# Performance work log

Measured on AMD Instinct MI355X. Metric: run time of the kernel, lower is better.

## Reference

```python
import jax, jax.numpy as jnp
import numpy as np

B, T, E, H = 16, 1024, 1024, 16
DH = E // H  # 64, divisible by 4
THETA = 10000.0


def setup_inputs() -> dict:
    key = jax.random.key(0)
    ks = jax.random.split(key, 10)
    inp = {
        "hidden_states": jax.random.normal(ks[0], (B, T, E), dtype=jnp.float32),
        "rope_pos": jax.random.randint(ks[1], (B, T, 2), 0, 32, dtype=jnp.int32),
    }
    s = 0.02
    inp["Wq"] = jax.random.normal(ks[2], (E, E), dtype=jnp.float32) * s
    inp["bq"] = jnp.zeros((E,), dtype=jnp.float32)
    inp["Wk"] = jax.random.normal(ks[3], (E, E), dtype=jnp.float32) * s
    inp["bk"] = jnp.zeros((E,), dtype=jnp.float32)
    inp["Wv"] = jax.random.normal(ks[4], (E, E), dtype=jnp.float32) * s
    inp["bv"] = jnp.zeros((E,), dtype=jnp.float32)
    inp["Wo"] = jax.random.normal(ks[5], (E, E), dtype=jnp.float32) * s
    inp["bo"] = jnp.zeros((E,), dtype=jnp.float32)
    return inp


def _rotate_half(x):
    # interleaved pairs: (x0,x1,x2,x3,...) -> (-x1,x0,-x3,x2,...)
    x_even = x[..., ::2]
    x_odd = x[..., 1::2]
    return jnp.stack((-x_odd, x_even), axis=-1).reshape(x.shape)


def _apply_rope_2d(q, k, rope_pos, theta):
    Dh = q.shape[-1]
    half, quarter = Dh // 2, Dh // 4
    dtype = q.dtype
    idx = jnp.arange(quarter, dtype=dtype)
    inv = (theta ** (-2.0 * idx / quarter)).astype(dtype)  # [quarter]
    pos_h = rope_pos[..., 0].astype(dtype)[..., None]  # [B,T,1]
    pos_w = rope_pos[..., 1].astype(dtype)[..., None]
    ang_h = pos_h * inv  # [B,T,quarter]
    ang_w = pos_w * inv
    ri = lambda a: jnp.repeat(a, 2, axis=-1)[:, None]  # -> [B,1,T,half]
    cos_h, sin_h = ri(jnp.cos(ang_h)), ri(jnp.sin(ang_h))
    cos_w, sin_w = ri(jnp.cos(ang_w)), ri(jnp.sin(ang_w))
    q_h, q_w = q[..., :half], q[..., half:]
    k_h, k_w = k[..., :half], k[..., half:]
    q_h = q_h * cos_h + _rotate_half(q_h) * sin_h
    k_h = k_h * cos_h + _rotate_half(k_h) * sin_h
    q_w = q_w * cos_w + _rotate_half(q_w) * sin_w
    k_w = k_w * cos_w + _rotate_half(k_w) * sin_w
    return jnp.concatenate([q_h, q_w], axis=-1), jnp.concatenate([k_h, k_w], axis=-1)


def reference(hidden_states, rope_pos, Wq, bq, Wk, bk, Wv, bv, Wo, bo):
    b, t, e = hidden_states.shape
    scale = DH ** -0.5
    # torch nn.Linear: y = x @ W.T + b, W is [out, in]
    proj = lambda x, W, bias: jnp.einsum('bte,oe->bto', x, W) + bias
    q = proj(hidden_states, Wq, bq).reshape(b, t, H, DH).transpose(0, 2, 1, 3)
    k = proj(hidden_states, Wk, bk).reshape(b, t, H, DH).transpose(0, 2, 1, 3)
    v = proj(hidden_states, Wv, bv).reshape(b, t, H, DH).transpose(0, 2, 1, 3)
    q, k = _apply_rope_2d(q, k, rope_pos, THETA)
    # eager attention: scores in input dtype, softmax in float32
    scores = jnp.einsum('bhqd,bhkd->bhqk', q, k) * scale
    w = jax.nn.softmax(scores.astype(jnp.float32), axis=-1).astype(q.dtype)
    out = jnp.einsum('bhqk,bhkd->bhqd', w, v)
    out = out.transpose(0, 2, 1, 3).reshape(b, t, e)
    return jnp.einsum('bte,oe->bto', out, Wo) + bo
```

## Files before the change

kernel.cpp:

```cpp
#include <hip/hip_runtime.h>
#include <hip/hip_bf16.h>

#define B_  16
#define T_  1024
#define E_  1024
#define H_  16
#define DH_ 64

typedef short s16x8 __attribute__((ext_vector_type(8)));
typedef float f32x4 __attribute__((ext_vector_type(4)));
typedef unsigned short u16x4 __attribute__((ext_vector_type(4)));

__device__ __forceinline__ void async_cp16(const void* g, void* l) {
  __builtin_amdgcn_global_load_lds(
      (__attribute__((address_space(1))) unsigned int*)(g),
      (__attribute__((address_space(3))) unsigned int*)(l), 16, 0, 0);
}

__device__ __forceinline__ s16x8 frag8(const void* p) { return *(const s16x8*)p; }

__device__ __forceinline__ float fexp2(float x) {
#if __has_builtin(__builtin_amdgcn_exp2f)
  return __builtin_amdgcn_exp2f(x);
#else
  return exp2f(x);
#endif
}

__device__ __forceinline__ unsigned short f2bu(float x) {
  __hip_bfloat16 h = __float2bfloat16(x);
  return *reinterpret_cast<unsigned short*>(&h);
}

__global__ __launch_bounds__(256) void cast_f32_bf16(const float* __restrict__ in,
                                                     __hip_bfloat16* __restrict__ out,
                                                     int n4) {
  int i = blockIdx.x * 256 + threadIdx.x;
  if (i >= n4) return;
  float4 v = ((const float4*)in)[i];
  __hip_bfloat16* o = out + (size_t)i * 4;
  o[0] = __float2bfloat16(v.x);
  o[1] = __float2bfloat16(v.y);
  o[2] = __float2bfloat16(v.z);
  o[3] = __float2bfloat16(v.w);
}

#define GEMM_CORE(A_, B_PTR_, K_)                                              \
  __shared__ __align__(16) __hip_bfloat16 As[128 * 64];                        \
  __shared__ __align__(16) __hip_bfloat16 Bs[128 * 64];                        \
  const int tid  = threadIdx.x;                                                \
  const int lane = tid & 63, wave = tid >> 6;                                  \
  const int col  = lane & 15, quad = lane >> 4;                                \
  const int wm = (wave >> 1) << 6, wn = (wave & 1) << 6;                       \
  const f32x4 fzero = {0.f, 0.f, 0.f, 0.f};                                    \
  f32x4 acc[4][4];                                                             \
  _Pragma("unroll") for (int i = 0; i < 4; i++)                                \
    _Pragma("unroll") for (int j = 0; j < 4; j++) acc[i][j] = fzero;           \
  const int r8 = lane >> 3;                                                    \
  const int kgs = (lane & 7) ^ (r8 & 7);                                       \
  const char* Asrc[4]; const char* Bsrc[4]; char* Adst[4]; char* Bdst[4];      \
  _Pragma("unroll") for (int u = 0; u < 4; u++) {                              \
    int ch = u * 4 + wave;                                                     \
    int row = ch * 8 + r8;                                                     \
    Asrc[u] = (const char*)(A_ + (size_t)(bm + row) * K_) + kgs * 16;          \
    Bsrc[u] = (const char*)(B_PTR_ + (size_t)(bn + row) * K_) + kgs * 16;      \
    Adst[u] = (char*)As + ch * 1024;                                           \
    Bdst[u] = (char*)Bs + ch * 1024;                                           \
  }                                                                            \
  const int sw0 = ((quad) ^ (col & 7)) * 16;                                   \
  const int sw1 = ((quad + 4) ^ (col & 7)) * 16;                               \
  for (int kt = 0; kt < (K_ >> 6); ++kt) {                                     \
    __syncthreads();                                                           \
    const int koff = kt * 128;                                                 \
    _Pragma("unroll") for (int u = 0; u < 4; u++) {                            \
      async_cp16(Asrc[u] + koff, Adst[u]);                                     \
      async_cp16(Bsrc[u] + koff, Bdst[u]);                                     \
    }                                                                          \
    __syncthreads();                                                           \
    s16x8 af[2][4], bf[2][4];                                                  \
    _Pragma("unroll") for (int i = 0; i < 4; i++) {                            \
      af[0][i] = frag8((const char*)As + (wm + i * 16 + col) * 128 + sw0);     \
      af[1][i] = frag8((const char*)As + (wm + i * 16 + col) * 128 + sw1);     \
    }                                                                          \
    _Pragma("unroll") for (int j = 0; j < 4; j++) {                            \
      bf[0][j] = frag8((const char*)Bs + (wn + j * 16 + col) * 128 + sw0);     \
      bf[1][j] = frag8((const char*)Bs + (wn + j * 16 + col) * 128 + sw1);     \
    }                                                                          \
    _Pragma("unroll") for (int i = 0; i < 4; i++)                              \
      _Pragma("unroll") for (int j = 0; j < 4; j++) {                          \
        acc[i][j] = __builtin_amdgcn_mfma_f32_16x16x32_bf16(af[0][i], bf[0][j], acc[i][j], 0, 0, 0); \
        acc[i][j] = __builtin_amdgcn_mfma_f32_16x16x32_bf16(af[1][i], bf[1][j], acc[i][j], 0, 0, 0); \
      }                                                                        \
  }

__global__ __launch_bounds__(256, 2) void gemm_qkv(const __hip_bfloat16* __restrict__ A,
                                                   const __hip_bfloat16* __restrict__ Wqkv,
                                                   const float* __restrict__ bq,
                                                   const float* __restrict__ bk,
                                                   const float* __restrict__ bv,
                                                   __hip_bfloat16* __restrict__ Qb,
                                                   __hip_bfloat16* __restrict__ Kb,
                                                   __hip_bfloat16* __restrict__ Vt) {
  const int bm = (blockIdx.x & 127) << 7;
  const int bn = (blockIdx.x >> 7) << 7;
  GEMM_CORE(A, Wqkv, 1024)

  const int seg = bn >> 10;
  const float* bp = (seg == 0) ? bq : (seg == 1) ? bk : bv;
  float bcol[4];
#pragma unroll
  for (int j = 0; j < 4; j++) bcol[j] = bp[(bn & 1023) + wn + j * 16 + col];
#pragma unroll
  for (int i = 0; i < 4; i++) {
#pragma unroll
    for (int j = 0; j < 4; j++) {
      const int nc = (bn & 1023) + wn + j * 16 + col;
#pragma unroll
      for (int r = 0; r < 4; r++) {
        const int grow = bm + wm + i * 16 + quad * 4 + r;
        float v = acc[i][j][r] + bcol[j];
        if (seg == 0) {
          Qb[(size_t)grow * 1024 + nc] = __float2bfloat16(v);
        } else if (seg == 1) {
          Kb[(size_t)grow * 1024 + nc] = __float2bfloat16(v);
        } else {
          int bb = grow >> 10, tt = grow & 1023;
          int hh = nc >> 6, dd = nc & 63;
          Vt[(((size_t)bb * H_ + hh) * DH_ + dd) * T_ + tt] = __float2bfloat16(v);
        }
      }
    }
  }
}

__global__ __launch_bounds__(256, 2) void gemm_out(const __hip_bfloat16* __restrict__ A,
                                                   const __hip_bfloat16* __restrict__ Bw,
                                                   const float* __restrict__ bias,
                                                   float* __restrict__ Cout) {
  const int bm = (blockIdx.x & 127) << 7;
  const int bn = (blockIdx.x >> 7) << 7;
  GEMM_CORE(A, Bw, 1024)

  float bcol[4];
#pragma unroll
  for (int j = 0; j < 4; j++) bcol[j] = bias[bn + wn + j * 16 + col];
#pragma unroll
  for (int i = 0; i < 4; i++)
#pragma unroll
    for (int j = 0; j < 4; j++) {
      const int gcol = bn + wn + j * 16 + col;
#pragma unroll
      for (int r = 0; r < 4; r++) {
        const int grow = bm + wm + i * 16 + quad * 4 + r;
        Cout[(size_t)grow * 1024 + gcol] = acc[i][j][r] + bcol[j];
      }
    }
}

__global__ __launch_bounds__(256) void rope2d(__hip_bfloat16* __restrict__ Q,
                                              __hip_bfloat16* __restrict__ K,
                                              const int* __restrict__ pos) {
  const int row = blockIdx.x;
  const int t   = threadIdx.x;
  const float ph = (float)pos[row * 2 + 0];
  const float pw = (float)pos[row * 2 + 1];
  const int pd = (2 * t) & 31;
  float cs[2], sn[2];
#pragma unroll
  for (int i = 0; i < 2; i++) {
    int pdi = pd + i;
    int f = pdi & 15;
    float p = (pdi & 16) ? pw : ph;
    float inv = __expf((float)f * (-1.1512925464970229f));
    float ang = p * inv;
    cs[i] = cosf(ang);
    sn[i] = sinf(ang);
  }
  const float QSC = 0.18033688011112043f;
  size_t base = (size_t)row * E_ + 4 * t;
  {
    __hip_bfloat16* P = Q;
    float e0 = __bfloat162float(P[base + 0]);
    float e1 = __bfloat162float(P[base + 1]);
    float e2 = __bfloat162float(P[base + 2]);
    float e3 = __bfloat162float(P[base + 3]);
    P[base + 0] = __float2bfloat16((e0 * cs[0] - e1 * sn[0]) * QSC);
    P[base + 1] = __float2bfloat16((e1 * cs[0] + e0 * sn[0]) * QSC);
    P[base + 2] = __float2bfloat16((e2 * cs[1] - e3 * sn[1]) * QSC);
    P[base + 3] = __float2bfloat16((e3 * cs[1] + e2 * sn[1]) * QSC);
  }
  {
    __hip_bfloat16* P = K;
    float e0 = __bfloat162float(P[base + 0]);
    float e1 = __bfloat162float(P[base + 1]);
    float e2 = __bfloat162float(P[base + 2]);
    float e3 = __bfloat162float(P[base + 3]);
    P[base + 0] = __float2bfloat16(e0 * cs[0] - e1 * sn[0]);
    P[base + 1] = __float2bfloat16(e1 * cs[0] + e0 * sn[0]);
    P[base + 2] = __float2bfloat16(e2 * cs[1] - e3 * sn[1]);
    P[base + 3] = __float2bfloat16(e3 * cs[1] + e2 * sn[1]);
  }
}

__global__ __launch_bounds__(256, 3) void attn_flash(const __hip_bfloat16* __restrict__ Q,
                                                     const __hip_bfloat16* __restrict__ Kt,
                                                     const __hip_bfloat16* __restrict__ Vt,
                                                     __hip_bfloat16* __restrict__ Oa) {
  __shared__ __align__(16) __hip_bfloat16 QP[128 * 72];
  __shared__ __align__(16) __hip_bfloat16 Ks[64 * 72];
  __shared__ __align__(16) __hip_bfloat16 Vs[64 * 72];

  const int bid = blockIdx.x;
  const int bh = bid >> 3;
  const int b = bh >> 4, h = bh & 15;
  const int qt = bid & 7;
  const int tid = threadIdx.x;
  const int lane = tid & 63, wave = tid >> 6;
  const int col = lane & 15, quad = lane >> 4;

  const size_t qrow0 = (size_t)b * T_ + qt * 128;

#pragma unroll
  for (int cc = 0; cc < 4; ++cc) {
    int c = tid + cc * 256;
    int r = c >> 3, k8 = c & 7;
    const float4* src = (const float4*)((const char*)(Q + (qrow0 + r) * E_ + h * DH_)) + k8;
    *(float4*)((char*)QP + r * 144 + k8 * 16) = *src;
  }

  const f32x4 fzero = {0.f, 0.f, 0.f, 0.f};
  f32x4 o[2][4];
  float lr[2] = {0.f, 0.f};
#pragma unroll
  for (int g = 0; g < 2; g++)
#pragma unroll
    for (int j = 0; j < 4; j++) o[g][j] = fzero;
  s16x8 qf[2][2];
  char* Pw = (char*)QP + wave * 32 * 144;

  for (int kt2 = 0; kt2 < 16; ++kt2) {
    __syncthreads();
    const int kb = kt2 * 64;
#pragma unroll
    for (int cc = 0; cc < 4; ++cc) {
      int c = tid + cc * 256;
      if (c < 512) {
        int r = c >> 3, k8 = c & 7;
        const float4* src = (const float4*)((const char*)(Kt + ((size_t)b * T_ + kb + r) * E_ + h * DH_)) + k8;
        *(float4*)((char*)Ks + r * 144 + k8 * 16) = *src;
      } else {
        int c2 = c - 512;
        int d = c2 >> 3, k8 = c2 & 7;
        const float4* src = (const float4*)((const char*)(Vt + (((size_t)b * H_ + h) * DH_ + d) * T_ + kb)) + k8;
        *(float4*)((char*)Vs + d * 144 + k8 * 16) = *src;
      }
    }
    __syncthreads();
    if (kt2 == 0) {
#pragma unroll
      for (int g = 0; g < 2; g++) {
        qf[g][0] = frag8((const char*)QP + (g * 64 + wave * 16 + col) * 144 + quad * 16);
        qf[g][1] = frag8((const char*)QP + (g * 64 + wave * 16 + col) * 144 + 64 + quad * 16);
      }
      __syncthreads();
    }
    s16x8 kf[4][2];
#pragma unroll
    for (int ktile = 0; ktile < 4; ktile++) {
      kf[ktile][0] = frag8((const char*)Ks + (ktile * 16 + col) * 144 + quad * 16);
      kf[ktile][1] = frag8((const char*)Ks + (ktile * 16 + col) * 144 + 64 + quad * 16);
    }
#pragma unroll
    for (int g = 0; g < 2; g++) {
#pragma unroll
      for (int ktile = 0; ktile < 4; ktile++) {
        f32x4 d = fzero;
        d = __builtin_amdgcn_mfma_f32_16x16x32_bf16(kf[ktile][0], qf[g][0], d, 0, 0, 0);
        d = __builtin_amdgcn_mfma_f32_16x16x32_bf16(kf[ktile][1], qf[g][1], d, 0, 0, 0);
        float p0 = fexp2(d[0]), p1 = fexp2(d[1]), p2 = fexp2(d[2]), p3 = fexp2(d[3]);
        lr[g] += (p0 + p1) + (p2 + p3);
        u16x4 pk = {f2bu(p0), f2bu(p1), f2bu(p2), f2bu(p3)};
        *(u16x4*)(Pw + (g * 16 + col) * 144 + ktile * 32 + quad * 8) = pk;
      }
    }
    s16x8 vf[4][2];
#pragma unroll
    for (int jm = 0; jm < 4; jm++) {
      vf[jm][0] = frag8((const char*)Vs + (jm * 16 + col) * 144 + quad * 16);
      vf[jm][1] = frag8((const char*)Vs + (jm * 16 + col) * 144 + 64 + quad * 16);
    }
#pragma unroll
    for (int g = 0; g < 2; g++) {
      s16x8 pf0 = frag8(Pw + (g * 16 + col) * 144 + quad * 16);
      s16x8 pf1 = frag8(Pw + (g * 16 + col) * 144 + 64 + quad * 16);
#pragma unroll
      for (int jm = 0; jm < 4; jm++) {
        o[g][jm] = __builtin_amdgcn_mfma_f32_16x16x32_bf16(vf[jm][0], pf0, o[g][jm], 0, 0, 0);
        o[g][jm] = __builtin_amdgcn_mfma_f32_16x16x32_bf16(vf[jm][1], pf1, o[g][jm], 0, 0, 0);
      }
    }
  }
#pragma unroll
  for (int g = 0; g < 2; g++) {
    lr[g] += __shfl_xor(lr[g], 16, 64);
    lr[g] += __shfl_xor(lr[g], 32, 64);
  }
#pragma unroll
  for (int g = 0; g < 2; g++) {
    float invl = 1.f / lr[g];
    size_t grow = qrow0 + g * 64 + wave * 16 + col;
    char* obase = (char*)(Oa + grow * E_ + h * DH_);
#pragma unroll
    for (int jm = 0; jm < 4; jm++) {
      u16x4 pk = {f2bu(o[g][jm][0] * invl), f2bu(o[g][jm][1] * invl),
                  f2bu(o[g][jm][2] * invl), f2bu(o[g][jm][3] * invl)};
      *(u16x4*)(obase + jm * 32 + quad * 8) = pk;
    }
  }
}

extern "C" void kernel_launch(void* const* d_in, const int* in_sizes, int n_in,
                              void* d_out, int out_size, void* d_ws, size_t ws_size,
                              hipStream_t stream) {
  const float* X   = (const float*)d_in[0];
  const int*   pos = (const int*)d_in[1];
  const float* Wq  = (const float*)d_in[2];
  const float* bq  = (const float*)d_in[3];
  const float* Wk  = (const float*)d_in[4];
  const float* bk  = (const float*)d_in[5];
  const float* Wv  = (const float*)d_in[6];
  const float* bv  = (const float*)d_in[7];
  const float* Wo  = (const float*)d_in[8];
  const float* bo  = (const float*)d_in[9];
  float* out = (float*)d_out;

  char* ws = (char*)d_ws;
  const size_t MB = 1024 * 1024;
  __hip_bfloat16* Xb    = (__hip_bfloat16*)(ws + 0 * MB);
  __hip_bfloat16* Qb    = (__hip_bfloat16*)(ws + 32 * MB);
  __hip_bfloat16* Kb    = (__hip_bfloat16*)(ws + 64 * MB);
  __hip_bfloat16* Vtb   = (__hip_bfloat16*)(ws + 96 * MB);
  __hip_bfloat16* Wqkvb = (__hip_bfloat16*)(ws + 128 * MB);
  __hip_bfloat16* Wob   = (__hip_bfloat16*)(ws + 136 * MB);
  __hip_bfloat16* Ab    = Xb;

  cast_f32_bf16<<<16384, 256, 0, stream>>>(X,  Xb,  4194304);
  cast_f32_bf16<<<1024,  256, 0, stream>>>(Wq, Wqkvb,           262144);
  cast_f32_bf16<<<1024,  256, 0, stream>>>(Wk, Wqkvb + 1048576, 262144);
  cast_f32_bf16<<<1024,  256, 0, stream>>>(Wv, Wqkvb + 2097152, 262144);
  cast_f32_bf16<<<1024,  256, 0, stream>>>(Wo, Wob,             262144);

  gemm_qkv<<<3072, 256, 0, stream>>>(Xb, Wqkvb, bq, bk, bv, Qb, Kb, Vtb);

  rope2d<<<16384, 256, 0, stream>>>(Qb, Kb, pos);
  attn_flash<<<2048, 256, 0, stream>>>(Qb, Kb, Vtb, Ab);

  gemm_out<<<1024, 256, 0, stream>>>(Ab, Wob, bo, out);
}
```

Before: 452.5 us.

## Rewrite projection GEMMs as 256x256 double-buffered 8-wave pipelined kernels

Replaces the 128x128 single-buffered GEMM core with a 256x256 tile, 512-thread kernel. It double-buffers in 128KB of LDS and interleaves async global->LDS loads with MFMA phases, using s_setprio and explicit vmcnt waits. Block indices are remapped across XCD-sized groups for better L2 locality. It also vectorizes the V-transpose stores, the cast kernel and the rope loads/stores, and uses __sincosf. The large LDS footprint and accumulator count reduce occupancy and raise register pressure, and the barrier-heavy schedule could stall if the loads are not hidden.

```diff
diff --git a/kernel.cpp b/kernel.cpp
--- a/kernel.cpp
+++ b/kernel.cpp
@@ -32,68 +32,119 @@
   return *reinterpret_cast<unsigned short*>(&h);
 }
 
+__device__ __forceinline__ float bu2f(unsigned short u) {
+  __hip_bfloat16 h = *reinterpret_cast<__hip_bfloat16*>(&u);
+  return __bfloat162float(h);
+}
+
 __global__ __launch_bounds__(256) void cast_f32_bf16(const float* __restrict__ in,
                                                      __hip_bfloat16* __restrict__ out,
                                                      int n4) {
   int i = blockIdx.x * 256 + threadIdx.x;
   if (i >= n4) return;
   float4 v = ((const float4*)in)[i];
-  __hip_bfloat16* o = out + (size_t)i * 4;
-  o[0] = __float2bfloat16(v.x);
-  o[1] = __float2bfloat16(v.y);
-  o[2] = __float2bfloat16(v.z);
-  o[3] = __float2bfloat16(v.w);
-}
-
-#define GEMM_CORE(A_, B_PTR_, K_)                                              \
-  __shared__ __align__(16) __hip_bfloat16 As[128 * 64];                        \
-  __shared__ __align__(16) __hip_bfloat16 Bs[128 * 64];                        \
-  const int tid  = threadIdx.x;                                                \
-  const int lane = tid & 63, wave = tid >> 6;                                  \
-  const int col  = lane & 15, quad = lane >> 4;                                \
-  const int wm = (wave >> 1) << 6, wn = (wave & 1) << 6;                       \
-  const f32x4 fzero = {0.f, 0.f, 0.f, 0.f};                                    \
-  f32x4 acc[4][4];                                                             \
-  _Pragma("unroll") for (int i = 0; i < 4; i++)                                \
-    _Pragma("unroll") for (int j = 0; j < 4; j++) acc[i][j] = fzero;           \
-  const int r8 = lane >> 3;                                                    \
-  const int kgs = (lane & 7) ^ (r8 & 7);                                       \
-  const char* Asrc[4]; const char* Bsrc[4]; char* Adst[4]; char* Bdst[4];      \
-  _Pragma("unroll") for (int u = 0; u < 4; u++) {                              \
-    int ch = u * 4 + wave;                                                     \
-    int row = ch * 8 + r8;                                                     \
-    Asrc[u] = (const char*)(A_ + (size_t)(bm + row) * K_) + kgs * 16;          \
-    Bsrc[u] = (const char*)(B_PTR_ + (size_t)(bn + row) * K_) + kgs * 16;      \
-    Adst[u] = (char*)As + ch * 1024;                                           \
-    Bdst[u] = (char*)Bs + ch * 1024;                                           \
-  }                                                                            \
-  const int sw0 = ((quad) ^ (col & 7)) * 16;                                   \
-  const int sw1 = ((quad + 4) ^ (col & 7)) * 16;                               \
-  for (int kt = 0; kt < (K_ >> 6); ++kt) {                                     \
-    __syncthreads();                                                           \
-    const int koff = kt * 128;                                                 \
-    _Pragma("unroll") for (int u = 0; u < 4; u++) {                            \
-      async_cp16(Asrc[u] + koff, Adst[u]);                                     \
-      async_cp16(Bsrc[u] + koff, Bdst[u]);                                     \
-    }                                                                          \
-    __syncthreads();                                                           \
-    s16x8 af[2][4], bf[2][4];                                                  \
-    _Pragma("unroll") for (int i = 0; i < 4; i++) {                            \
-      af[0][i] = frag8((const char*)As + (wm + i * 16 + col) * 128 + sw0);     \
-      af[1][i] = frag8((const char*)As + (wm + i * 16 + col) * 128 + sw1);     \
-    }                                                                          \
-    _Pragma("unroll") for (int j = 0; j < 4; j++) {                            \
-      bf[0][j] = frag8((const char*)Bs + (wn + j * 16 + col) * 128 + sw0);     \
-      bf[1][j] = frag8((const char*)Bs + (wn + j * 16 + col) * 128 + sw1);     \
-    }                                                                          \
-    _Pragma("unroll") for (int i = 0; i < 4; i++)                              \
-      _Pragma("unroll") for (int j = 0; j < 4; j++) {                          \
-        acc[i][j] = __builtin_amdgcn_mfma_f32_16x16x32_bf16(af[0][i], bf[0][j], acc[i][j], 0, 0, 0); \
-        acc[i][j] = __builtin_amdgcn_mfma_f32_16x16x32_bf16(af[1][i], bf[1][j], acc[i][j], 0, 0, 0); \
-      }                                                                        \
-  }
-
-__global__ __launch_bounds__(256, 2) void gemm_qkv(const __hip_bfloat16* __restrict__ A,
+  u16x4 pk = {f2bu(v.x), f2bu(v.y), f2bu(v.z), f2bu(v.w)};
+  *(u16x4*)(out + (size_t)i * 4) = pk;
+}
+
+#define G8_ISSUE(SRC_, LOFF_, H_, D_, KT_)                                      \
+  {                                                                             \
+    _Pragma("unroll") for (int u_ = 0; u_ < 2; ++u_) {                          \
+      const int ch_ = u_ * 8 + wave;                                            \
+      async_cp16(SRC_ + (size_t)((H_)*128 + ch_ * 8) * 2048 + (KT_)*128,        \
+                 smem + (D_)*65536 + (LOFF_) + (H_)*16384 + ch_ * 1024);        \
+    }                                                                           \
+  }
+
+#define G8_READ_A(D_, S_)                                                       \
+  {                                                                             \
+    _Pragma("unroll") for (int i_ = 0; i_ < 4; ++i_) {                          \
+      const char* rp_ = smem + (D_)*65536 + wrow * 16384 +                      \
+                        ((S_)*64 + i_ * 16 + col) * 128;                        \
+      af[i_][0] = frag8(rp_ + sw0);                                             \
+      af[i_][1] = frag8(rp_ + sw1);                                             \
+    }                                                                           \
+  }
+
+#define G8_READ_B(D_, T8_, BF_)                                                 \
+  {                                                                             \
+    _Pragma("unroll") for (int j_ = 0; j_ < 2; ++j_) {                          \
+      const char* rp_ = smem + (D_)*65536 + 32768 + (wcol >> 1) * 16384 +       \
+                        ((wcol & 1) * 64 + (T8_)*32 + j_ * 16 + col) * 128;     \
+      BF_[j_][0] = frag8(rp_ + sw0);                                            \
+      BF_[j_][1] = frag8(rp_ + sw1);                                            \
+    }                                                                           \
+  }
+
+#define G8_MFMA(S_, T8_, BF_)                                                   \
+  {                                                                             \
+    __builtin_amdgcn_s_setprio(1);                                              \
+    _Pragma("unroll") for (int i_ = 0; i_ < 4; ++i_)                            \
+      _Pragma("unroll") for (int j_ = 0; j_ < 2; ++j_) {                        \
+        acc[(S_)*4 + i_][(T8_)*2 + j_] = __builtin_amdgcn_mfma_f32_16x16x32_bf16( \
+            af[i_][0], BF_[j_][0], acc[(S_)*4 + i_][(T8_)*2 + j_], 0, 0, 0);    \
+        acc[(S_)*4 + i_][(T8_)*2 + j_] = __builtin_amdgcn_mfma_f32_16x16x32_bf16( \
+            af[i_][1], BF_[j_][1], acc[(S_)*4 + i_][(T8_)*2 + j_], 0, 0, 0);    \
+      }                                                                         \
+    __builtin_amdgcn_s_setprio(0);                                              \
+  }
+
+#define G8_KTILE(D_, GA_, GB_, KTA_, KTB_, VM_)                                 \
+  G8_READ_A(D_, 0)                                                              \
+  G8_READ_B(D_, 0, bf0)                                                         \
+  if (GA_) G8_ISSUE(Asrc, 0, 0, (D_) ^ 1, KTA_)                                 \
+  __builtin_amdgcn_s_barrier();                                                 \
+  G8_MFMA(0, 0, bf0)                                                            \
+  __builtin_amdgcn_s_barrier();                                                 \
+  G8_READ_B(D_, 1, bf1)                                                         \
+  if (GA_) G8_ISSUE(Asrc, 0, 1, (D_) ^ 1, KTA_)                                 \
+  __builtin_amdgcn_s_barrier();                                                 \
+  G8_MFMA(0, 1, bf1)                                                            \
+  __builtin_amdgcn_s_barrier();                                                 \
+  G8_READ_A(D_, 1)                                                              \
+  if (GB_) G8_ISSUE(Bsrc, 32768, 0, (D_), KTB_)                                 \
+  __builtin_amdgcn_s_barrier();                                                 \
+  G8_MFMA(1, 1, bf1)                                                            \
+  __builtin_amdgcn_s_barrier();                                                 \
+  if (GB_) G8_ISSUE(Bsrc, 32768, 1, (D_), KTB_)                                 \
+  __builtin_amdgcn_s_barrier();                                                 \
+  G8_MFMA(1, 0, bf0)                                                            \
+  if (VM_) { asm volatile("s_waitcnt vmcnt(4)" ::: "memory"); }                 \
+  else     { asm volatile("s_waitcnt vmcnt(0)" ::: "memory"); }                 \
+  __builtin_amdgcn_s_barrier();
+
+#define G8_CORE(APTR_, BPTR_)                                                   \
+  __shared__ __align__(16) char smem[131072];                                   \
+  const int tid = threadIdx.x;                                                  \
+  const int lane = tid & 63, wave = tid >> 6;                                   \
+  const int col = lane & 15, quad = lane >> 4;                                  \
+  const int wrow = wave >> 2, wcol = wave & 3;                                  \
+  const int r8 = lane >> 3;                                                     \
+  const int gsw = (lane & 7) ^ r8;                                              \
+  const int sw0 = (quad ^ (col & 7)) * 16;                                      \
+  const int sw1 = ((quad + 4) ^ (col & 7)) * 16;                                \
+  const char* Asrc = (const char*)(APTR_) + (size_t)(bm + r8) * 2048 + gsw * 16;\
+  const char* Bsrc = (const char*)(BPTR_) + (size_t)(bn + r8) * 2048 + gsw * 16;\
+  const f32x4 fzero = {0.f, 0.f, 0.f, 0.f};                                     \
+  f32x4 acc[8][4];                                                              \
+  _Pragma("unroll") for (int i_ = 0; i_ < 8; i_++)                              \
+    _Pragma("unroll") for (int j_ = 0; j_ < 4; j_++) acc[i_][j_] = fzero;       \
+  s16x8 af[4][2], bf0[2][2], bf1[2][2];                                         \
+  G8_ISSUE(Bsrc, 32768, 0, 0, 0)                                                \
+  G8_ISSUE(Bsrc, 32768, 1, 0, 0)                                                \
+  G8_ISSUE(Asrc, 0, 0, 0, 0)                                                    \
+  G8_ISSUE(Asrc, 0, 1, 0, 0)                                                    \
+  G8_ISSUE(Bsrc, 32768, 0, 1, 1)                                                \
+  G8_ISSUE(Bsrc, 32768, 1, 1, 1)                                                \
+  asm volatile("s_waitcnt vmcnt(4)" ::: "memory");                              \
+  __builtin_amdgcn_s_barrier();                                                 \
+  _Pragma("clang loop unroll(disable)") for (int it = 0; it < 8; ++it) {        \
+    const bool g7 = (it < 7);                                                   \
+    G8_KTILE(0, true, g7, 2 * it + 1, 2 * it + 2, g7)                           \
+    G8_KTILE(1, g7, g7, 2 * it + 2, 2 * it + 3, g7)                             \
+  }
+
+__global__ __launch_bounds__(512, 2) void gemm_qkv(const __hip_bfloat16* __restrict__ A,
                                                    const __hip_bfloat16* __restrict__ Wqkv,
                                                    const float* __restrict__ bq,
                                                    const float* __restrict__ bk,
@@ -101,60 +152,71 @@
                                                    __hip_bfloat16* __restrict__ Qb,
                                                    __hip_bfloat16* __restrict__ Kb,
                                                    __hip_bfloat16* __restrict__ Vt) {
-  const int bm = (blockIdx.x & 127) << 7;
-  const int bn = (blockIdx.x >> 7) << 7;
-  GEMM_CORE(A, Wqkv, 1024)
+  const int wg = (blockIdx.x & 7) * 96 + (blockIdx.x >> 3);
+  const int bm = (wg & 63) << 8;
+  const int bn = (wg >> 6) << 8;
+  G8_CORE(A, Wqkv)
 
   const int seg = bn >> 10;
   const float* bp = (seg == 0) ? bq : (seg == 1) ? bk : bv;
+  const int nbase = (bn & 1023) + wcol * 64;
   float bcol[4];
 #pragma unroll
-  for (int j = 0; j < 4; j++) bcol[j] = bp[(bn & 1023) + wn + j * 16 + col];
-#pragma unroll
-  for (int i = 0; i < 4; i++) {
-#pragma unroll
-    for (int j = 0; j < 4; j++) {
-      const int nc = (bn & 1023) + wn + j * 16 + col;
-#pragma unroll
-      for (int r = 0; r < 4; r++) {
-        const int grow = bm + wm + i * 16 + quad * 4 + r;
-        float v = acc[i][j][r] + bcol[j];
-        if (seg == 0) {
-          Qb[(size_t)grow * 1024 + nc] = __float2bfloat16(v);
-        } else if (seg == 1) {
-          Kb[(size_t)grow * 1024 + nc] = __float2bfloat16(v);
-        } else {
-          int bb = grow >> 10, tt = grow & 1023;
-          int hh = nc >> 6, dd = nc & 63;
-          Vt[(((size_t)bb * H_ + hh) * DH_ + dd) * T_ + tt] = __float2bfloat16(v);
-        }
-      }
-    }
-  }
-}
-
-__global__ __launch_bounds__(256, 2) void gemm_out(const __hip_bfloat16* __restrict__ A,
+  for (int j = 0; j < 4; j++) bcol[j] = bp[nbase + j * 16 + col];
+  if (seg < 2) {
+    __hip_bfloat16* P = (seg == 0) ? Qb : Kb;
+#pragma unroll
+    for (int mi = 0; mi < 8; mi++) {
+      const int gr0 = bm + wrow * 128 + mi * 16 + quad * 4;
+#pragma unroll
+      for (int ni = 0; ni < 4; ni++) {
+        const int nc = nbase + ni * 16 + col;
+#pragma unroll
+        for (int r = 0; r < 4; r++)
+          P[(size_t)(gr0 + r) * 1024 + nc] = __float2bfloat16(acc[mi][ni][r] + bcol[ni]);
+      }
+    }
+  } else {
+#pragma unroll
+    for (int mi = 0; mi < 8; mi++) {
+      const int gr0 = bm + wrow * 128 + mi * 16 + quad * 4;
+      const int bb = gr0 >> 10, tt = gr0 & 1023;
+#pragma unroll
+      for (int ni = 0; ni < 4; ni++) {
+        const int nc = nbase + ni * 16 + col;
+        const int hh = nc >> 6, dd = nc & 63;
+        u16x4 pk = {f2bu(acc[mi][ni][0] + bcol[ni]), f2bu(acc[mi][ni][1] + bcol[ni]),
+                    f2bu(acc[mi][ni][2] + bcol[ni]), f2bu(acc[mi][ni][3] + bcol[ni])};
+        *(u16x4*)(Vt + (((size_t)bb * H_ + hh) * DH_ + dd) * T_ + tt) = pk;
+      }
+    }
+  }
+}
+
+__global__ __launch_bounds__(512, 2) void gemm_out(const __hip_bfloat16* __restrict__ A,
                                                    const __hip_bfloat16* __restrict__ Bw,
                                                    const float* __restrict__ bias,
                                                    float* __restrict__ Cout) {
-  const int bm = (blockIdx.x & 127) << 7;
-  const int bn = (blockIdx.x >> 7) << 7;
-  GEMM_CORE(A, Bw, 1024)
-
+  const int wg = (blockIdx.x & 7) * 32 + (blockIdx.x >> 3);
+  const int bm = (wg & 63) << 8;
+  const int bn = (wg >> 6) << 8;
+  G8_CORE(A, Bw)
+
+  const int nbase = bn + wcol * 64;
   float bcol[4];
 #pragma unroll
-  for (int j = 0; j < 4; j++) bcol[j] = bias[bn + wn + j * 16 + col];
-#pragma unroll
-  for (int i = 0; i < 4; i++)
-#pragma unroll
-    for (int j = 0; j < 4; j++) {
-      const int gcol = bn + wn + j * 16 + col;
-#pragma unroll
-      for (int r = 0; r < 4; r++) {
-        const int grow = bm + wm + i * 16 + quad * 4 + r;
-        Cout[(size_t)grow * 1024 + gcol] = acc[i][j][r] + bcol[j];
-      }
-    }
+  for (int j = 0; j < 4; j++) bcol[j] = bias[nbase + j * 16 + col];
+#pragma unroll
+  for (int mi = 0; mi < 8; mi++) {
+    const int gr0 = bm + wrow * 128 + mi * 16 + quad * 4;
+#pragma unroll
+    for (int ni = 0; ni < 4; ni++) {
+      const int gcol = nbase + ni * 16 + col;
+#pragma unroll
+      for (int r = 0; r < 4; r++)
+        Cout[(size_t)(gr0 + r) * 1024 + gcol] = acc[mi][ni][r] + bcol[ni];
+    }
+  }
 }
 
 __global__ __launch_bounds__(256) void rope2d(__hip_bfloat16* __restrict__ Q,
@@ -173,32 +235,27 @@
     float p = (pdi & 16) ? pw : ph;
     float inv = __expf((float)f * (-1.1512925464970229f));
     float ang = p * inv;
-    cs[i] = cosf(ang);
-    sn[i] = sinf(ang);
+    __sincosf(ang, &sn[i], &cs[i]);
   }
   const float QSC = 0.18033688011112043f;
   size_t base = (size_t)row * E_ + 4 * t;
   {
-    __hip_bfloat16* P = Q;
-    float e0 = __bfloat162float(P[base + 0]);
-    float e1 = __bfloat162float(P[base + 1]);
-    float e2 = __bfloat162float(P[base + 2]);
-    float e3 = __bfloat162float(P[base + 3]);
-    P[base + 0] = __float2bfloat16((e0 * cs[0] - e1 * sn[0]) * QSC);
-    P[base + 1] = __float2bfloat16((e1 * cs[0] + e0 * sn[0]) * QSC);
-    P[base + 2] = __float2bfloat16((e2 * cs[1] - e3 * sn[1]) * QSC);
-    P[base + 3] = __float2bfloat16((e3 * cs[1] + e2 * sn[1]) * QSC);
+    u16x4 q4 = *(u16x4*)(Q + base);
+    float e0 = bu2f(q4[0]), e1 = bu2f(q4[1]), e2 = bu2f(q4[2]), e3 = bu2f(q4[3]);
+    u16x4 o4 = {f2bu((e0 * cs[0] - e1 * sn[0]) * QSC),
+                f2bu((e1 * cs[0] + e0 * sn[0]) * QSC),
+                f2bu((e2 * cs[1] - e3 * sn[1]) * QSC),
+                f2bu((e3 * cs[1] + e2 * sn[1]) * QSC)};
+    *(u16x4*)(Q + base) = o4;
   }
   {
-    __hip_bfloat16* P = K;
-    float e0 = __bfloat162float(P[base + 0]);
-    float e1 = __bfloat162float(P[base + 1]);
-    float e2 = __bfloat162float(P[base + 2]);
-    float e3 = __bfloat162float(P[base + 3]);
-    P[base + 0] = __float2bfloat16(e0 * cs[0] - e1 * sn[0]);
-    P[base + 1] = __float2bfloat16(e1 * cs[0] + e0 * sn[0]);
-    P[base + 2] = __float2bfloat16(e2 * cs[1] - e3 * sn[1]);
-    P[base + 3] = __float2bfloat16(e3 * cs[1] + e2 * sn[1]);
+    u16x4 k4 = *(u16x4*)(K + base);
+    float e0 = bu2f(k4[0]), e1 = bu2f(k4[1]), e2 = bu2f(k4[2]), e3 = bu2f(k4[3]);
+    u16x4 o4 = {f2bu(e0 * cs[0] - e1 * sn[0]),
+                f2bu(e1 * cs[0] + e0 * sn[0]),
+                f2bu(e2 * cs[1] - e3 * sn[1]),
+                f2bu(e3 * cs[1] + e2 * sn[1])};
+    *(u16x4*)(K + base) = o4;
   }
 }
 
@@ -350,10 +407,10 @@
   cast_f32_bf16<<<1024,  256, 0, stream>>>(Wv, Wqkvb + 2097152, 262144);
   cast_f32_bf16<<<1024,  256, 0, stream>>>(Wo, Wob,             262144);
 
-  gemm_qkv<<<3072, 256, 0, stream>>>(Xb, Wqkvb, bq, bk, bv, Qb, Kb, Vtb);
+  gemm_qkv<<<768, 512, 0, stream>>>(Xb, Wqkvb, bq, bk, bv, Qb, Kb, Vtb);
 
   rope2d<<<16384, 256, 0, stream>>>(Qb, Kb, pos);
   attn_flash<<<2048, 256, 0, stream>>>(Qb, Kb, Vtb, Ab);
 
-  gemm_out<<<1024, 256, 0, stream>>>(Ab, Wob, bo, out);
-}
+  gemm_out<<<256, 512, 0, stream>>>(Ab, Wob, bo, out);
+}
```

Measured after the change: 446.7 us. No clear change (-1.3%).
